# Optimization experiments

Hardware: AMD Instinct MI355X
Metric: run time of the kernel (lower is better)

The kernel has to match this reference:

```python
import jax, jax.numpy as jnp
import numpy as np

N_NODES = 100000
N_EDGES = 1600000
C_IN = 128
C_OUT = 64
BN_EPS = 1e-5
LEAKY_SLOPE = 0.01


def setup_inputs() -> dict:
    key = jax.random.key(0)
    k1, k2, k3 = jax.random.split(key, 3)
    x = jax.random.normal(k1, (N_NODES, C_IN), dtype=jnp.float32)
    edge_index = jax.random.randint(k2, (2, N_EDGES), 0, N_NODES, dtype=jnp.int32)
    W = jax.random.normal(k3, (C_IN, C_OUT), dtype=jnp.float32) * (1.0 / np.sqrt(C_IN))
    b = jnp.zeros((C_OUT,), dtype=jnp.float32)
    gamma = jnp.ones((C_OUT,), dtype=jnp.float32)
    beta = jnp.zeros((C_OUT,), dtype=jnp.float32)
    return {"x": x, "edge_index": edge_index, "W": W, "b": b, "gamma": gamma, "beta": beta}


def reference(x, edge_index, W, b, gamma, beta):
    n = x.shape[0]
    # --- GCNConv: add self-loops, symmetric normalization ---
    loop = jnp.arange(n, dtype=edge_index.dtype)
    row = jnp.concatenate([edge_index[0], loop])  # source
    col = jnp.concatenate([edge_index[1], loop])  # target
    deg = jax.ops.segment_sum(jnp.ones_like(col, dtype=x.dtype), col, num_segments=n)
    deg_inv_sqrt = jnp.where(deg > 0, jax.lax.rsqrt(deg), 0.0)
    norm = deg_inv_sqrt[row] * deg_inv_sqrt[col]  # [E+N]
    xw = x @ W  # [N, C_OUT] - transform before aggregation (PyG GCNConv)
    msgs = xw[row] * norm[:, None]  # [E+N, C_OUT]
    out = jax.ops.segment_sum(msgs, col, num_segments=n) + b  # [N, C_OUT]
    # --- BatchNorm (training mode: batch stats over nodes, biased var) ---
    mean = jnp.mean(out, axis=0)
    var = jnp.mean(jnp.square(out - mean), axis=0)
    y = gamma * (out - mean) * jax.lax.rsqrt(var + BN_EPS) + beta
    # --- LeakyReLU (default negative_slope=0.01); dropout p=0 is identity ---
    return jnp.where(y >= 0, y, LEAKY_SLOPE * y)
```

## Files before the change

kernel.cpp:

```cpp
#include <hip/hip_runtime.h>

#define C_IN 128
#define C_OUT 64
#define BN_EPS 1e-5f
#define LEAKY 0.01f

#define BSZ   256
#define NBMAX 512
#define CAP   6144
#define CHUNKA 4096

using bf16x8 = __attribute__((ext_vector_type(8))) __bf16;
using f32x4  = __attribute__((ext_vector_type(4))) float;

__device__ inline unsigned short f2b(float f) {
    unsigned u = __float_as_uint(f);
    return (unsigned short)((u + 0x7fffu + ((u >> 16) & 1u)) >> 16);
}
__device__ inline float b2f(unsigned short b) {
    return __uint_as_float(((unsigned)b) << 16);
}

__global__ __launch_bounds__(256) void k_binA(const int* __restrict__ rows,
                                              const int* __restrict__ cols,
                                              int* __restrict__ bfill,
                                              unsigned* __restrict__ pairs,
                                              int nE, int NB) {
    __shared__ int hist[NBMAX];
    __shared__ int base[NBMAX];
    int t = threadIdx.x;
    int chunk = blockIdx.x * CHUNKA;
    int e = min(chunk + CHUNKA, nE);

    for (int b = t; b < NB; b += 256) hist[b] = 0;
    __syncthreads();

    for (int i = chunk + t; i < e; i += 256)
        atomicAdd(&hist[cols[i] >> 8], 1);
    __syncthreads();

    for (int b = t; b < NB; b += 256) {
        int cnt = hist[b];
        base[b] = cnt ? atomicAdd(&bfill[b], cnt) : 0;
        hist[b] = 0;
    }
    __syncthreads();

    for (int i = chunk + t; i < e; i += 256) {
        int c = cols[i];
        unsigned r = (unsigned)rows[i];
        int b = c >> 8;
        int off = base[b] + atomicAdd(&hist[b], 1);
        if (off < CAP)
            pairs[(size_t)b * CAP + off] = ((unsigned)(c & (BSZ - 1)) << 24) | r;
    }
}

__global__ __launch_bounds__(512) void k_bucket_scan(const int* __restrict__ bfill,
                                                     int* __restrict__ sbase, int NB) {
    __shared__ int s[512];
    int t = threadIdx.x;
    int v = (t < NB) ? bfill[t] : 0;
    s[t] = v;
    __syncthreads();
    for (int off = 1; off < 512; off <<= 1) {
        int x = (t >= off) ? s[t - off] : 0;
        __syncthreads();
        s[t] += x;
        __syncthreads();
    }
    if (t < NB) sbase[t] = s[t] - v;
}

__global__ __launch_bounds__(256) void k_binB(const int* __restrict__ bfill,
                                              const int* __restrict__ sbase,
                                              const unsigned* __restrict__ pairs,
                                              int* __restrict__ deg,
                                              int* __restrict__ ptr,
                                              int* __restrict__ srcs, int n) {
    __shared__ unsigned rowbuf[CAP];
    __shared__ int sorted[CAP];
    __shared__ int histL[BSZ];
    __shared__ int scanL[BSZ];
    int b = blockIdx.x;
    int t = threadIdx.x;
    int cnt = min(bfill[b], CAP);
    const unsigned* reg = pairs + (size_t)b * CAP;

    histL[t] = 0;
    __syncthreads();
    for (int i = t; i < cnt; i += 256) {
        unsigned p = reg[i];
        rowbuf[i] = p;
        atomicAdd(&histL[p >> 24], 1);
    }
    __syncthreads();

    int hv = histL[t];
    scanL[t] = hv;
    __syncthreads();
    for (int off = 1; off < 256; off <<= 1) {
        int x = (t >= off) ? scanL[t - off] : 0;
        __syncthreads();
        scanL[t] += x;
        __syncthreads();
    }
    int my_start = scanL[t] - hv;

    int s0 = sbase[b];
    int node = (b << 8) + t;
    if (node < n) {
        deg[node] = hv;
        ptr[node] = s0 + my_start;
    }
    __syncthreads();
    histL[t] = my_start;
    __syncthreads();
    for (int i = t; i < cnt; i += 256) {
        unsigned p = rowbuf[i];
        int pos = atomicAdd(&histL[p >> 24], 1);
        sorted[pos] = (int)(p & 0xFFFFFFu);
    }
    __syncthreads();
    for (int i = t; i < cnt; i += 256)
        srcs[s0 + i] = sorted[i];
}

__global__ __launch_bounds__(256) void k_dis(const int* __restrict__ deg,
                                             float* __restrict__ dis, int n) {
    int i = blockIdx.x * 256 + threadIdx.x;
    if (i < n) dis[i] = rsqrtf((float)(deg[i] + 1));
}

__global__ __launch_bounds__(256) void k_wprep(const float* __restrict__ W,
                                               unsigned short* __restrict__ wb) {
    int idx = blockIdx.x * 256 + threadIdx.x;
    if (idx >= C_IN * C_OUT) return;
    int k = idx >> 6, col = idx & 63;
    int t = col >> 4, nlo = col & 15;
    int c = k >> 5, q = (k >> 3) & 3, j = k & 7;
    wb[(size_t)((((t * 4 + c) * 4 + q) * 16) + nlo) * 8 + j] = f2b(W[idx]);
}

__global__ __launch_bounds__(256) void k_gemm(const float* __restrict__ x,
                                              const unsigned short* __restrict__ wb,
                                              const float* __restrict__ dis,
                                              unsigned short* __restrict__ xwsb, int n) {
    const int lane = threadIdx.x & 63;
    const int wave = threadIdx.x >> 6;
    const int base = (blockIdx.x * 4 + wave) * 16;
    if (base >= n) return;

    const int nlo  = lane & 15;
    const int quad = lane >> 4;

    const bf16x8* Wv = (const bf16x8*)wb;
    bf16x8 Bf[4][4];
    #pragma unroll
    for (int t = 0; t < 4; ++t)
        #pragma unroll
        for (int c = 0; c < 4; ++c)
            Bf[t][c] = Wv[((t * 4 + c) * 4 + quad) * 16 + nlo];

    f32x4 acc[4] = {};
    int m = base + nlo;
    const float* xrow = x + (size_t)(m < n ? m : n - 1) * C_IN;

    #pragma unroll
    for (int c = 0; c < 4; ++c) {
        float4 a0 = *(const float4*)&xrow[c * 32 + quad * 8];
        float4 a1 = *(const float4*)&xrow[c * 32 + quad * 8 + 4];
        bf16x8 Af;
        Af[0] = (__bf16)a0.x; Af[1] = (__bf16)a0.y;
        Af[2] = (__bf16)a0.z; Af[3] = (__bf16)a0.w;
        Af[4] = (__bf16)a1.x; Af[5] = (__bf16)a1.y;
        Af[6] = (__bf16)a1.z; Af[7] = (__bf16)a1.w;
        #pragma unroll
        for (int t = 0; t < 4; ++t)
            acc[t] = __builtin_amdgcn_mfma_f32_16x16x32_bf16(Af, Bf[t][c], acc[t], 0, 0, 0);
    }

    #pragma unroll
    for (int r = 0; r < 4; ++r) {
        int node = base + quad * 4 + r;
        if (node < n) {
            float dn = dis[node];
            #pragma unroll
            for (int t = 0; t < 4; ++t)
                xwsb[(size_t)node * C_OUT + t * 16 + nlo] = f2b(acc[t][r] * dn);
        }
    }
}

__global__ __launch_bounds__(256) void k_gather(const int* __restrict__ ptr,
                                                const int* __restrict__ deg,
                                                const int* __restrict__ srcs,
                                                const unsigned short* __restrict__ xwsb,
                                                float* __restrict__ out,
                                                const float* __restrict__ dis, int n) {
    int lane = threadIdx.x & 63;
    int node = blockIdx.x * 4 + (threadIdx.x >> 6);
    if (node >= n) return;
    int s = lane & 7;
    int g = lane >> 3;

    int start = ptr[node];
    int dg = deg[node];
    float dn = dis[node];

    float acc[8] = {0.f, 0.f, 0.f, 0.f, 0.f, 0.f, 0.f, 0.f};
    const uint4* xw16 = (const uint4*)xwsb;

    for (int b = 0; b < dg; b += 64) {
        int m = min(64, dg - b);
        int sv = (lane < m) ? srcs[start + b + lane] : 0;
        #pragma unroll
        for (int j = 0; j < 8; ++j) {
            int idx = j * 8 + g;
            int src = __shfl(sv, idx);
            if (idx < m) {
                uint4 d = xw16[(size_t)src * 8 + s];
                acc[0] += __uint_as_float(d.x << 16);
                acc[1] += __uint_as_float(d.x & 0xffff0000u);
                acc[2] += __uint_as_float(d.y << 16);
                acc[3] += __uint_as_float(d.y & 0xffff0000u);
                acc[4] += __uint_as_float(d.z << 16);
                acc[5] += __uint_as_float(d.z & 0xffff0000u);
                acc[6] += __uint_as_float(d.w << 16);
                acc[7] += __uint_as_float(d.w & 0xffff0000u);
            }
        }
    }

    #pragma unroll
    for (int k = 0; k < 4; ++k) {
        float send = (lane & 8) ? acc[k] : acc[k + 4];
        float recv = __shfl_xor(send, 8);
        acc[k] = ((lane & 8) ? acc[k + 4] : acc[k]) + recv;
    }
    #pragma unroll
    for (int k = 0; k < 2; ++k) {
        float send = (lane & 16) ? acc[k] : acc[k + 2];
        float recv = __shfl_xor(send, 16);
        acc[k] = ((lane & 16) ? acc[k + 2] : acc[k]) + recv;
    }
    {
        float send = (lane & 32) ? acc[0] : acc[1];
        float recv = __shfl_xor(send, 32);
        acc[0] = ((lane & 32) ? acc[1] : acc[0]) + recv;
    }
    int c = s * 8 + ((lane & 8) ? 4 : 0) + ((lane & 16) ? 2 : 0) + ((lane & 32) ? 1 : 0);

    float v = acc[0] + b2f(xwsb[(size_t)node * C_OUT + c]);
    out[(size_t)node * C_OUT + c] = v * dn;
}

__global__ __launch_bounds__(256) void k_stats(const float* __restrict__ agg,
                                               float* __restrict__ stats, int n) {
    int c = threadIdx.x & 63;
    int sub = threadIdx.x >> 6;
    float s = 0.f, s2 = 0.f;
    for (int node = blockIdx.x * 4 + sub; node < n; node += gridDim.x * 4) {
        float v = agg[(size_t)node * C_OUT + c];
        s += v;
        s2 += v * v;
    }
    __shared__ float red[2][4][64];
    red[0][sub][c] = s;
    red[1][sub][c] = s2;
    __syncthreads();
    if (sub == 0) {
        s  = red[0][0][c] + red[0][1][c] + red[0][2][c] + red[0][3][c];
        s2 = red[1][0][c] + red[1][1][c] + red[1][2][c] + red[1][3][c];
        atomicAdd(&stats[c], s);
        atomicAdd(&stats[64 + c], s2);
    }
}

__global__ __launch_bounds__(256) void k_final(const float* __restrict__ stats,
                                               const float* __restrict__ gamma,
                                               const float* __restrict__ beta,
                                               float* __restrict__ out, int n) {
    int gid = blockIdx.x * 256 + threadIdx.x;
    int total4 = n * (C_OUT / 4);
    if (gid >= total4) return;
    int c4 = (gid & 15) * 4;
    float inv_n = 1.0f / (float)n;
    float4 s  = *(const float4*)&stats[c4];
    float4 s2 = *(const float4*)&stats[64 + c4];
    float4 g4 = *(const float4*)&gamma[c4];
    float4 b4 = *(const float4*)&beta[c4];
    float4 v = ((const float4*)out)[gid];

    float m, var, k, y;
    m = s.x * inv_n; var = s2.x * inv_n - m * m; k = rsqrtf(var + BN_EPS) * g4.x;
    y = (v.x - m) * k + b4.x; v.x = y >= 0.f ? y : LEAKY * y;
    m = s.y * inv_n; var = s2.y * inv_n - m * m; k = rsqrtf(var + BN_EPS) * g4.y;
    y = (v.y - m) * k + b4.y; v.y = y >= 0.f ? y : LEAKY * y;
    m = s.z * inv_n; var = s2.z * inv_n - m * m; k = rsqrtf(var + BN_EPS) * g4.z;
    y = (v.z - m) * k + b4.z; v.z = y >= 0.f ? y : LEAKY * y;
    m = s.w * inv_n; var = s2.w * inv_n - m * m; k = rsqrtf(var + BN_EPS) * g4.w;
    y = (v.w - m) * k + b4.w; v.w = y >= 0.f ? y : LEAKY * y;

    ((float4*)out)[gid] = v;
}

extern "C" void kernel_launch(void* const* d_in, const int* in_sizes, int n_in,
                              void* d_out, int out_size, void* d_ws, size_t ws_size,
                              hipStream_t stream) {
    const float* x     = (const float*)d_in[0];
    const int*   ei    = (const int*)d_in[1];
    const float* W     = (const float*)d_in[2];
    const float* gamma = (const float*)d_in[4];
    const float* beta  = (const float*)d_in[5];
    float* out = (float*)d_out;

    int n  = in_sizes[0] / C_IN;
    int nE = in_sizes[1] / 2;
    const int* rows = ei;
    const int* cols = ei + nE;
    int NB = (n + BSZ - 1) / BSZ;

    int*   deg   = (int*)d_ws;
    int*   ptr   = deg + n;
    float* dis   = (float*)(ptr + n);
    unsigned short* xwsb = (unsigned short*)(dis + n);
    int*   srcs  = (int*)((float*)(dis + n) + (size_t)n * (C_OUT / 2));
    unsigned* pairs = (unsigned*)(srcs + nE);
    int*   bfill = (int*)(pairs + (size_t)NB * CAP);
    int*   sbase = bfill + NBMAX;
    float* stats = (float*)(sbase + NBMAX);
    unsigned short* wb = (unsigned short*)(stats + 2 * C_OUT);

    hipMemsetAsync(bfill, 0, NBMAX * sizeof(int), stream);
    hipMemsetAsync(stats, 0, 2 * C_OUT * sizeof(float), stream);

    k_binA<<<(nE + CHUNKA - 1) / CHUNKA, 256, 0, stream>>>(rows, cols, bfill, pairs, nE, NB);
    k_bucket_scan<<<1, 512, 0, stream>>>(bfill, sbase, NB);
    k_binB<<<NB, 256, 0, stream>>>(bfill, sbase, pairs, deg, ptr, srcs, n);

    k_dis<<<(n + 255) / 256, 256, 0, stream>>>(deg, dis, n);
    k_wprep<<<(C_IN * C_OUT + 255) / 256, 256, 0, stream>>>(W, wb);
    k_gemm<<<(n + 63) / 64, 256, 0, stream>>>(x, wb, dis, xwsb, n);

    k_gather<<<(n + 3) / 4, 256, 0, stream>>>(ptr, deg, srcs, xwsb, out, dis, n);

    k_stats<<<512, 256, 0, stream>>>(out, stats, n);
    k_final<<<(n * (C_OUT / 4) + 255) / 256, 256, 0, stream>>>(stats, gamma, beta, out, n);
}
```

Before: 233.1 us.

## Fuse GCN pipeline stages, drop bucket scan, fold BN stats into gather

The number of launches drops. Memsets are folded into a combined W-prep/zero kernel, and the bucket scan is removed by writing sorted sources in place into each bucket's fixed-capacity region. Degree and pointer are packed into one int2, and the separate rsqrt-degree kernel is replaced by inline computation. The gather becomes a grid-stride kernel that prefetches the next node's metadata and accumulates the BatchNorm sum and sum of squares, which removes the separate stats pass over the output. The edge-binning chunk size is also halved. The risks are fewer gather blocks limiting latency hiding, and stats atomics now depending on the gather grid size.

```diff
diff --git a/kernel.cpp b/kernel.cpp
--- a/kernel.cpp
+++ b/kernel.cpp
@@ -8,7 +8,7 @@
 #define BSZ   256
 #define NBMAX 512
 #define CAP   6144
-#define CHUNKA 4096
+#define CHUNKA 2048
 
 using bf16x8 = __attribute__((ext_vector_type(8))) __bf16;
 using f32x4  = __attribute__((ext_vector_type(4))) float;
@@ -19,6 +19,20 @@
 }
 __device__ inline float b2f(unsigned short b) {
     return __uint_as_float(((unsigned)b) << 16);
+}
+
+__global__ __launch_bounds__(256) void k_prep(const float* __restrict__ W,
+                                              unsigned short* __restrict__ wb,
+                                              int* __restrict__ bfill,
+                                              float* __restrict__ stats) {
+    int idx = blockIdx.x * 256 + threadIdx.x;
+    if (idx < NBMAX) bfill[idx] = 0;
+    if (idx >= NBMAX && idx < NBMAX + 2 * C_OUT) stats[idx - NBMAX] = 0.f;
+    if (idx >= C_IN * C_OUT) return;
+    int k = idx >> 6, col = idx & 63;
+    int t = col >> 4, nlo = col & 15;
+    int c = k >> 5, q = (k >> 3) & 3, j = k & 7;
+    wb[(size_t)((((t * 4 + c) * 4 + q) * 16) + nlo) * 8 + j] = f2b(W[idx]);
 }
 
 __global__ __launch_bounds__(256) void k_binA(const int* __restrict__ rows,
@@ -56,27 +70,9 @@
     }
 }
 
-__global__ __launch_bounds__(512) void k_bucket_scan(const int* __restrict__ bfill,
-                                                     int* __restrict__ sbase, int NB) {
-    __shared__ int s[512];
-    int t = threadIdx.x;
-    int v = (t < NB) ? bfill[t] : 0;
-    s[t] = v;
-    __syncthreads();
-    for (int off = 1; off < 512; off <<= 1) {
-        int x = (t >= off) ? s[t - off] : 0;
-        __syncthreads();
-        s[t] += x;
-        __syncthreads();
-    }
-    if (t < NB) sbase[t] = s[t] - v;
-}
-
 __global__ __launch_bounds__(256) void k_binB(const int* __restrict__ bfill,
-                                              const int* __restrict__ sbase,
                                               const unsigned* __restrict__ pairs,
-                                              int* __restrict__ deg,
-                                              int* __restrict__ ptr,
+                                              int2* __restrict__ pd,
                                               int* __restrict__ srcs, int n) {
     __shared__ unsigned rowbuf[CAP];
     __shared__ int sorted[CAP];
@@ -107,12 +103,9 @@
     }
     int my_start = scanL[t] - hv;
 
-    int s0 = sbase[b];
+    int s0 = b * CAP;
     int node = (b << 8) + t;
-    if (node < n) {
-        deg[node] = hv;
-        ptr[node] = s0 + my_start;
-    }
+    if (node < n) pd[node] = make_int2(s0 + my_start, hv);
     __syncthreads();
     histL[t] = my_start;
     __syncthreads();
@@ -126,25 +119,9 @@
         srcs[s0 + i] = sorted[i];
 }
 
-__global__ __launch_bounds__(256) void k_dis(const int* __restrict__ deg,
-                                             float* __restrict__ dis, int n) {
-    int i = blockIdx.x * 256 + threadIdx.x;
-    if (i < n) dis[i] = rsqrtf((float)(deg[i] + 1));
-}
-
-__global__ __launch_bounds__(256) void k_wprep(const float* __restrict__ W,
-                                               unsigned short* __restrict__ wb) {
-    int idx = blockIdx.x * 256 + threadIdx.x;
-    if (idx >= C_IN * C_OUT) return;
-    int k = idx >> 6, col = idx & 63;
-    int t = col >> 4, nlo = col & 15;
-    int c = k >> 5, q = (k >> 3) & 3, j = k & 7;
-    wb[(size_t)((((t * 4 + c) * 4 + q) * 16) + nlo) * 8 + j] = f2b(W[idx]);
-}
-
 __global__ __launch_bounds__(256) void k_gemm(const float* __restrict__ x,
                                               const unsigned short* __restrict__ wb,
-                                              const float* __restrict__ dis,
+                                              const int2* __restrict__ pd,
                                               unsigned short* __restrict__ xwsb, int n) {
     const int lane = threadIdx.x & 63;
     const int wave = threadIdx.x >> 6;
@@ -184,7 +161,7 @@
     for (int r = 0; r < 4; ++r) {
         int node = base + quad * 4 + r;
         if (node < n) {
-            float dn = dis[node];
+            float dn = rsqrtf((float)(pd[node].y + 1));
             #pragma unroll
             for (int t = 0; t < 4; ++t)
                 xwsb[(size_t)node * C_OUT + t * 16 + nlo] = f2b(acc[t][r] * dn);
@@ -192,88 +169,120 @@
     }
 }
 
-__global__ __launch_bounds__(256) void k_gather(const int* __restrict__ ptr,
-                                                const int* __restrict__ deg,
+#define ACC8(d) do { \
+    acc[0] += __uint_as_float((d).x << 16); \
+    acc[1] += __uint_as_float((d).x & 0xffff0000u); \
+    acc[2] += __uint_as_float((d).y << 16); \
+    acc[3] += __uint_as_float((d).y & 0xffff0000u); \
+    acc[4] += __uint_as_float((d).z << 16); \
+    acc[5] += __uint_as_float((d).z & 0xffff0000u); \
+    acc[6] += __uint_as_float((d).w << 16); \
+    acc[7] += __uint_as_float((d).w & 0xffff0000u); } while (0)
+
+__global__ __launch_bounds__(256) void k_gather(const int2* __restrict__ pd,
                                                 const int* __restrict__ srcs,
                                                 const unsigned short* __restrict__ xwsb,
                                                 float* __restrict__ out,
-                                                const float* __restrict__ dis, int n) {
+                                                float* __restrict__ stats, int n) {
     int lane = threadIdx.x & 63;
-    int node = blockIdx.x * 4 + (threadIdx.x >> 6);
-    if (node >= n) return;
+    int wv = threadIdx.x >> 6;
     int s = lane & 7;
     int g = lane >> 3;
-
-    int start = ptr[node];
-    int dg = deg[node];
-    float dn = dis[node];
-
-    float acc[8] = {0.f, 0.f, 0.f, 0.f, 0.f, 0.f, 0.f, 0.f};
+    int c = s * 8 + ((lane & 8) ? 4 : 0) + ((lane & 16) ? 2 : 0) + ((lane & 32) ? 1 : 0);
     const uint4* xw16 = (const uint4*)xwsb;
-
-    for (int b = 0; b < dg; b += 64) {
-        int m = min(64, dg - b);
-        int sv = (lane < m) ? srcs[start + b + lane] : 0;
+    int stride = gridDim.x * 4;
+
+    float ssum = 0.f, ssq = 0.f;
+
+    int node = blockIdx.x * 4 + wv;
+    int2 p = (node < n) ? pd[node] : make_int2(0, 0);
+    int sv = (node < n && lane < p.y) ? srcs[p.x + lane] : 0;
+    float selfv = (node < n) ? b2f(xwsb[(size_t)node * C_OUT + c]) : 0.f;
+
+    while (node < n) {
+        int nxt = node + stride;
+        int2 pn = make_int2(0, 0);
+        int svn = 0;
+        float selfn = 0.f;
+        if (nxt < n) {
+            pn = pd[nxt];
+            svn = (lane < pn.y) ? srcs[pn.x + lane] : 0;
+            selfn = b2f(xwsb[(size_t)nxt * C_OUT + c]);
+        }
+
+        int dg = p.y;
+        float dn = rsqrtf((float)(dg + 1));
+        float acc[8] = {0.f, 0.f, 0.f, 0.f, 0.f, 0.f, 0.f, 0.f};
+
+        int m0 = min(dg, 64);
+        int full = m0 >> 3;
+        for (int j = 0; j < full; ++j) {
+            int src = __shfl(sv, j * 8 + g);
+            uint4 d = xw16[(src << 3) + s];
+            ACC8(d);
+        }
+        if (m0 & 7) {
+            int idx = full * 8 + g;
+            int src = __shfl(sv, idx);
+            if (idx < m0) {
+                uint4 d = xw16[(src << 3) + s];
+                ACC8(d);
+            }
+        }
+        for (int b2 = 64; b2 < dg; b2 += 64) {
+            int m = min(64, dg - b2);
+            int sv2 = (lane < m) ? srcs[p.x + b2 + lane] : 0;
+            int f2 = m >> 3;
+            for (int j = 0; j < f2; ++j) {
+                int src = __shfl(sv2, j * 8 + g);
+                uint4 d = xw16[(src << 3) + s];
+                ACC8(d);
+            }
+            if (m & 7) {
+                int idx = f2 * 8 + g;
+                int src = __shfl(sv2, idx);
+                if (idx < m) {
+                    uint4 d = xw16[(src << 3) + s];
+                    ACC8(d);
+                }
+            }
+        }
+
         #pragma unroll
-        for (int j = 0; j < 8; ++j) {
-            int idx = j * 8 + g;
-            int src = __shfl(sv, idx);
-            if (idx < m) {
-                uint4 d = xw16[(size_t)src * 8 + s];
-                acc[0] += __uint_as_float(d.x << 16);
-                acc[1] += __uint_as_float(d.x & 0xffff0000u);
-                acc[2] += __uint_as_float(d.y << 16);
-                acc[3] += __uint_as_float(d.y & 0xffff0000u);
-                acc[4] += __uint_as_float(d.z << 16);
-                acc[5] += __uint_as_float(d.z & 0xffff0000u);
-                acc[6] += __uint_as_float(d.w << 16);
-                acc[7] += __uint_as_float(d.w & 0xffff0000u);
-            }
-        }
-    }
-
-    #pragma unroll
-    for (int k = 0; k < 4; ++k) {
-        float send = (lane & 8) ? acc[k] : acc[k + 4];
-        float recv = __shfl_xor(send, 8);
-        acc[k] = ((lane & 8) ? acc[k + 4] : acc[k]) + recv;
-    }
-    #pragma unroll
-    for (int k = 0; k < 2; ++k) {
-        float send = (lane & 16) ? acc[k] : acc[k + 2];
-        float recv = __shfl_xor(send, 16);
-        acc[k] = ((lane & 16) ? acc[k + 2] : acc[k]) + recv;
-    }
-    {
-        float send = (lane & 32) ? acc[0] : acc[1];
-        float recv = __shfl_xor(send, 32);
-        acc[0] = ((lane & 32) ? acc[1] : acc[0]) + recv;
-    }
-    int c = s * 8 + ((lane & 8) ? 4 : 0) + ((lane & 16) ? 2 : 0) + ((lane & 32) ? 1 : 0);
-
-    float v = acc[0] + b2f(xwsb[(size_t)node * C_OUT + c]);
-    out[(size_t)node * C_OUT + c] = v * dn;
-}
-
-__global__ __launch_bounds__(256) void k_stats(const float* __restrict__ agg,
-                                               float* __restrict__ stats, int n) {
-    int c = threadIdx.x & 63;
-    int sub = threadIdx.x >> 6;
-    float s = 0.f, s2 = 0.f;
-    for (int node = blockIdx.x * 4 + sub; node < n; node += gridDim.x * 4) {
-        float v = agg[(size_t)node * C_OUT + c];
-        s += v;
-        s2 += v * v;
-    }
+        for (int k = 0; k < 4; ++k) {
+            float send = (lane & 8) ? acc[k] : acc[k + 4];
+            float recv = __shfl_xor(send, 8);
+            acc[k] = ((lane & 8) ? acc[k + 4] : acc[k]) + recv;
+        }
+        #pragma unroll
+        for (int k = 0; k < 2; ++k) {
+            float send = (lane & 16) ? acc[k] : acc[k + 2];
+            float recv = __shfl_xor(send, 16);
+            acc[k] = ((lane & 16) ? acc[k + 2] : acc[k]) + recv;
+        }
+        {
+            float send = (lane & 32) ? acc[0] : acc[1];
+            float recv = __shfl_xor(send, 32);
+            acc[0] = ((lane & 32) ? acc[1] : acc[0]) + recv;
+        }
+
+        float v = (acc[0] + selfv) * dn;
+        out[(size_t)node * C_OUT + c] = v;
+        ssum += v;
+        ssq += v * v;
+
+        node = nxt; p = pn; sv = svn; selfv = selfn;
+    }
+
     __shared__ float red[2][4][64];
-    red[0][sub][c] = s;
-    red[1][sub][c] = s2;
-    __syncthreads();
-    if (sub == 0) {
-        s  = red[0][0][c] + red[0][1][c] + red[0][2][c] + red[0][3][c];
-        s2 = red[1][0][c] + red[1][1][c] + red[1][2][c] + red[1][3][c];
-        atomicAdd(&stats[c], s);
-        atomicAdd(&stats[64 + c], s2);
+    red[0][wv][c] = ssum;
+    red[1][wv][c] = ssq;
+    __syncthreads();
+    if (wv == 0) {
+        float a = red[0][0][c] + red[0][1][c] + red[0][2][c] + red[0][3][c];
+        float q = red[1][0][c] + red[1][1][c] + red[1][2][c] + red[1][3][c];
+        atomicAdd(&stats[c], a);
+        atomicAdd(&stats[C_OUT + c], q);
     }
 }
 
@@ -321,30 +330,18 @@
     const int* cols = ei + nE;
     int NB = (n + BSZ - 1) / BSZ;
 
-    int*   deg   = (int*)d_ws;
-    int*   ptr   = deg + n;
-    float* dis   = (float*)(ptr + n);
-    unsigned short* xwsb = (unsigned short*)(dis + n);
-    int*   srcs  = (int*)((float*)(dis + n) + (size_t)n * (C_OUT / 2));
-    unsigned* pairs = (unsigned*)(srcs + nE);
-    int*   bfill = (int*)(pairs + (size_t)NB * CAP);
-    int*   sbase = bfill + NBMAX;
-    float* stats = (float*)(sbase + NBMAX);
+    int2* pd = (int2*)d_ws;
+    unsigned short* xwsb = (unsigned short*)(pd + n);
+    unsigned* pairs = (unsigned*)(xwsb + (size_t)n * C_OUT);
+    int* srcs = (int*)pairs;
+    int* bfill = (int*)(pairs + (size_t)NB * CAP);
+    float* stats = (float*)(bfill + NBMAX);
     unsigned short* wb = (unsigned short*)(stats + 2 * C_OUT);
 
-    hipMemsetAsync(bfill, 0, NBMAX * sizeof(int), stream);
-    hipMemsetAsync(stats, 0, 2 * C_OUT * sizeof(float), stream);
-
+    k_prep<<<(C_IN * C_OUT + 255) / 256, 256, 0, stream>>>(W, wb, bfill, stats);
     k_binA<<<(nE + CHUNKA - 1) / CHUNKA, 256, 0, stream>>>(rows, cols, bfill, pairs, nE, NB);
-    k_bucket_scan<<<1, 512, 0, stream>>>(bfill, sbase, NB);
-    k_binB<<<NB, 256, 0, stream>>>(bfill, sbase, pairs, deg, ptr, srcs, n);
-
-    k_dis<<<(n + 255) / 256, 256, 0, stream>>>(deg, dis, n);
-    k_wprep<<<(C_IN * C_OUT + 255) / 256, 256, 0, stream>>>(W, wb);
-    k_gemm<<<(n + 63) / 64, 256, 0, stream>>>(x, wb, dis, xwsb, n);
-
-    k_gather<<<(n + 3) / 4, 256, 0, stream>>>(ptr, deg, srcs, xwsb, out, dis, n);
-
-    k_stats<<<512, 256, 0, stream>>>(out, stats, n);
+    k_binB<<<NB, 256, 0, stream>>>(bfill, pairs, pd, srcs, n);
+    k_gemm<<<(n + 63) / 64, 256, 0, stream>>>(x, wb, pd, xwsb, n);
+    k_gather<<<2048, 256, 0, stream>>>(pd, srcs, xwsb, out, stats, n);
     k_final<<<(n * (C_OUT / 4) + 255) / 256, 256, 0, stream>>>(stats, gamma, beta, out, n);
 }
```

Result: slower. 240.2 us (+3.0%).
